# Kernel tuning notes

Hardware: AMD Instinct MI355X
Metric: run time of the kernel (lower is better)

The kernel has to match this reference:

```python
import jax, jax.numpy as jnp
import numpy as np
import itertools

NUM_HEADS = 8
KEY_DIM = 32
ATTN_D = 128  # attn_ratio * key_dim
BN_EPS = 1e-5


def _build_idxs(rx=16, rz=8, tn=1):
    points = list(itertools.product(range(rx), range(rx)))
    for i in range(tn):
        points += list(itertools.product(range(rx + rz * i, rx + rz * (i + 1)),
                                         range(rx + rz * i, rx + rz * (i + 1))))
    offsets = {}
    idxs = []
    for p1 in points:
        for p2 in points:
            off = (abs(p1[0] - p2[0]), abs(p1[1] - p2[1]))
            if off not in offsets:
                offsets[off] = len(offsets)
            idxs.append(offsets[off])
    N = len(points)
    return np.asarray(idxs, dtype=np.int64).reshape(N, N), len(offsets)


def _bn_train(x2d, gamma, beta):
    # BatchNorm1d in training mode: batch mean / biased variance over dim 0
    m = jnp.mean(x2d, axis=0)
    v = jnp.var(x2d, axis=0)
    return (x2d - m) * jax.lax.rsqrt(v + BN_EPS) * gamma + beta


def setup_inputs() -> dict:
    key = jax.random.key(0)
    ks = jax.random.split(key, 4)
    idxs_np, n_off = _build_idxs()  # (320,320), 560
    B, N, C = 128, idxs_np.shape[0], 256
    h = NUM_HEADS * (2 * KEY_DIM + ATTN_D)  # 1536
    dh = NUM_HEADS * ATTN_D  # 1024
    return {
        "x": jax.random.normal(ks[0], (B, N, C), dtype=jnp.float32),
        "Wqkv": jax.random.normal(ks[1], (h, C), dtype=jnp.float32) * 0.02,
        "g1": jnp.ones((h,), jnp.float32),
        "b1": jnp.zeros((h,), jnp.float32),
        "ab": jax.random.normal(ks[2], (NUM_HEADS, n_off), dtype=jnp.float32) * 0.02,
        "Wproj": jax.random.normal(ks[3], (C, dh), dtype=jnp.float32) * 0.02,
        "g2": jnp.ones((C,), jnp.float32),
        "b2": jnp.zeros((C,), jnp.float32),
        "idxs": jnp.asarray(idxs_np),
    }


def reference(x, Wqkv, g1, b1, ab, Wproj, g2, b2, idxs):
    B, N, C = x.shape
    scale = KEY_DIM ** -0.5
    # qkv projection (Linear no-bias) + BatchNorm1d over flattened (B*N, h)
    qkv = jnp.einsum('bnc,hc->bnh', x, Wqkv)
    qkv = _bn_train(qkv.reshape(B * N, -1), g1, b1).reshape(B, N, NUM_HEADS, 2 * KEY_DIM + ATTN_D)
    q = qkv[..., :KEY_DIM]
    k = qkv[..., KEY_DIM:2 * KEY_DIM]
    v = qkv[..., 2 * KEY_DIM:]
    bias = ab[:, idxs]  # gather -> (H, N, N)
    attn = jnp.einsum('bnhd,bmhd->bhnm', q, k) * scale + bias[None]
    attn = jax.nn.softmax(attn, axis=-1)
    out = jnp.einsum('bhnm,bmhd->bnhd', attn, v).reshape(B, N, NUM_HEADS * ATTN_D)
    out = jax.nn.gelu(out, approximate=False)  # activation() before proj
    out = jnp.einsum('bnd,cd->bnc', out, Wproj)
    out = _bn_train(out.reshape(B * N, -1), g2, b2).reshape(B, N, C)
    return out
```

## Files before the change

### kernel.cpp

```cpp
#include <hip/hip_runtime.h>
#include <hip/hip_bf16.h>

#define B_ 128
#define N_ 320
#define C_ 256
#define H_ 8
#define HQKV 1536
#define DH 1024
#define MROWS 40960
#define EPS 1e-5f
#define SCALE 0.17677669529663687f
#define LOG2E 1.4426950408889634f

typedef __attribute__((ext_vector_type(4))) float f32x4;
typedef __attribute__((ext_vector_type(8))) short short8_t;
typedef __attribute__((ext_vector_type(4))) short short4_t;

__device__ inline float bf2f(unsigned short u) { return __uint_as_float(((unsigned)u) << 16); }
__device__ inline unsigned short f2bf(float f) {
    unsigned u = __float_as_uint(f);
    u += 0x7FFF + ((u >> 16) & 1);
    return (unsigned short)(u >> 16);
}

__device__ inline float gelu_f(float v) {
    float v2 = v * v;
    float w = fmaf(v2, 0.044715f, 1.0f);
    float z = v * w * (-2.3022098f);
    float e = __builtin_amdgcn_exp2f(z);
    return v * __builtin_amdgcn_rcpf(1.0f + e);
}

#define GLD16(gp, lp)                                                                  \
    __builtin_amdgcn_global_load_lds((const __attribute__((address_space(1))) void*)(gp), \
                                     (__attribute__((address_space(3))) void*)(lp), 16, 0, 0)

__global__ void conv_all(const float* __restrict__ x, const float* __restrict__ wqkv,
                         const float* __restrict__ wproj, unsigned short* __restrict__ xb,
                         unsigned short* __restrict__ wqb, unsigned short* __restrict__ wpb) {
    int i = blockIdx.x * 256 + threadIdx.x;
    const float* src;
    unsigned short* dst;
    int off;
    if (i < 2621440) { src = x; dst = xb; off = i; }
    else if (i < 2719744) { src = wqkv; dst = wqb; off = i - 2621440; }
    else if (i < 2785280) { src = wproj; dst = wpb; off = i - 2719744; }
    else return;
    f32x4 v = ((const f32x4*)src)[off];
    short4_t o;
#pragma unroll
    for (int j = 0; j < 4; ++j) o[j] = (short)f2bf(v[j]);
    ((short4_t*)dst)[off] = o;
}

__global__ __launch_bounds__(256) void gemm_qkv(const unsigned short* __restrict__ A,
                                                const unsigned short* __restrict__ Bm,
                                                unsigned short* __restrict__ qkB,
                                                unsigned short* __restrict__ vT,
                                                float* __restrict__ sum1, float* __restrict__ sumsq1) {
    __shared__ unsigned short lA[128 * 32];
    __shared__ unsigned short lB[128 * 32];
    const int tid = threadIdx.x;
    const int lane = tid & 63, wid = tid >> 6;
    const int wm = wid >> 1, wn = wid & 1;
    const int lr = lane & 15, g = lane >> 4, lk = g * 8;
    const int m0 = blockIdx.y * 128, n0 = blockIdx.x * 128;
    const int wb0 = tid & 192;
    f32x4 acc[4][4] = {};
    for (int k0 = 0; k0 < 256; k0 += 32) {
        __syncthreads();
#pragma unroll
        for (int j = 0; j < 2; ++j) {
            int idx = j * 256 + tid;
            int wb = j * 256 + wb0;
            GLD16(&A[(size_t)(m0 + (idx >> 2)) * 256 + k0 + (idx & 3) * 8], &lA[(size_t)wb * 8]);
            GLD16(&Bm[(size_t)(n0 + (idx >> 2)) * 256 + k0 + (idx & 3) * 8], &lB[(size_t)wb * 8]);
        }
        __syncthreads();
        short8_t af[4], bfr[4];
#pragma unroll
        for (int i = 0; i < 4; ++i) af[i] = *(short8_t*)&lA[(wm * 64 + i * 16 + lr) * 32 + lk];
#pragma unroll
        for (int j = 0; j < 4; ++j) bfr[j] = *(short8_t*)&lB[(wn * 64 + j * 16 + lr) * 32 + lk];
#pragma unroll
        for (int i = 0; i < 4; ++i)
#pragma unroll
            for (int j = 0; j < 4; ++j)
                acc[i][j] = __builtin_amdgcn_mfma_f32_16x16x32_bf16(af[i], bfr[j], acc[i][j], 0, 0, 0);
    }
    int hhj[4], cmj[4];
#pragma unroll
    for (int j = 0; j < 4; ++j) {
        int col = n0 + wn * 64 + j * 16 + lr;
        hhj[j] = col / 192;
        cmj[j] = col - hhj[j] * 192;
    }
    float cs[4] = {0.f, 0.f, 0.f, 0.f}, css[4] = {0.f, 0.f, 0.f, 0.f};
#pragma unroll
    for (int i = 0; i < 4; ++i) {
        int rowbase = m0 + wm * 64 + i * 16 + g * 4;
        int bq = rowbase / 320;
        int n = rowbase - bq * 320;
#pragma unroll
        for (int j = 0; j < 4; ++j) {
            float v0 = acc[i][j][0], v1 = acc[i][j][1], v2 = acc[i][j][2], v3 = acc[i][j][3];
            cs[j] += (v0 + v1) + (v2 + v3);
            css[j] += (v0 * v0 + v1 * v1) + (v2 * v2 + v3 * v3);
            if (cmj[j] < 64) {
                unsigned short* qp = &qkB[((size_t)(bq * 8 + hhj[j]) * 320 + n) * 64 + cmj[j]];
                qp[0] = f2bf(v0); qp[64] = f2bf(v1); qp[128] = f2bf(v2); qp[192] = f2bf(v3);
            } else {
                short4_t o;
                o[0] = (short)f2bf(v0); o[1] = (short)f2bf(v1);
                o[2] = (short)f2bf(v2); o[3] = (short)f2bf(v3);
                *(short4_t*)&vT[((size_t)(bq * 8 + hhj[j]) * 128 + (cmj[j] - 64)) * 320 + n] = o;
            }
        }
    }
    __syncthreads();
    float* red_s = (float*)lA;
    float* red_ss = (float*)lB;
#pragma unroll
    for (int j = 0; j < 4; ++j) {
        int c = wn * 64 + j * 16 + lr;
        red_s[(wm * 4 + g) * 128 + c] = cs[j];
        red_ss[(wm * 4 + g) * 128 + c] = css[j];
    }
    __syncthreads();
    if (tid < 128) {
        float s = 0.f;
#pragma unroll
        for (int u = 0; u < 8; ++u) s += red_s[u * 128 + tid];
        atomicAdd(&sum1[n0 + tid], s);
    } else {
        int c = tid - 128;
        float s = 0.f;
#pragma unroll
        for (int u = 0; u < 8; ++u) s += red_ss[u * 128 + c];
        atomicAdd(&sumsq1[n0 + c], s);
    }
}

__global__ __launch_bounds__(256) void gemm_proj(const unsigned short* __restrict__ A,
                                                 const unsigned short* __restrict__ Bm,
                                                 float* __restrict__ Cout,
                                                 float* __restrict__ sum2, float* __restrict__ sumsq2) {
    __shared__ unsigned short lA[64 * 32];
    __shared__ unsigned short lB[128 * 32];
    const int tid = threadIdx.x;
    const int lane = tid & 63, wid = tid >> 6;
    const int wm = wid >> 1, wn = wid & 1;
    const int lr = lane & 15, g = lane >> 4, lk = g * 8;
    const int m0 = blockIdx.y * 64, n0 = blockIdx.x * 128;
    const int wb0 = tid & 192;
    f32x4 acc[2][4] = {};
    for (int k0 = 0; k0 < 1024; k0 += 32) {
        __syncthreads();
        GLD16(&A[(size_t)(m0 + (tid >> 2)) * 1024 + k0 + (tid & 3) * 8], &lA[(size_t)wb0 * 8]);
        GLD16(&Bm[(size_t)(n0 + (tid >> 2)) * 1024 + k0 + (tid & 3) * 8], &lB[(size_t)wb0 * 8]);
        GLD16(&Bm[(size_t)(n0 + 64 + (tid >> 2)) * 1024 + k0 + (tid & 3) * 8], &lB[2048 + (size_t)wb0 * 8]);
        __syncthreads();
        short8_t af[2], bfr[4];
#pragma unroll
        for (int i = 0; i < 2; ++i) af[i] = *(short8_t*)&lA[(wm * 32 + i * 16 + lr) * 32 + lk];
#pragma unroll
        for (int j = 0; j < 4; ++j) bfr[j] = *(short8_t*)&lB[(wn * 64 + j * 16 + lr) * 32 + lk];
#pragma unroll
        for (int i = 0; i < 2; ++i)
#pragma unroll
            for (int j = 0; j < 4; ++j)
                acc[i][j] = __builtin_amdgcn_mfma_f32_16x16x32_bf16(af[i], bfr[j], acc[i][j], 0, 0, 0);
    }
    float cs[4] = {0.f, 0.f, 0.f, 0.f}, css[4] = {0.f, 0.f, 0.f, 0.f};
#pragma unroll
    for (int i = 0; i < 2; ++i) {
#pragma unroll
        for (int r = 0; r < 4; ++r) {
            int row = m0 + wm * 32 + i * 16 + g * 4 + r;
#pragma unroll
            for (int j = 0; j < 4; ++j) {
                float val = acc[i][j][r];
                cs[j] += val;
                css[j] += val * val;
                Cout[(size_t)row * 256 + n0 + wn * 64 + j * 16 + lr] = val;
            }
        }
    }
    __syncthreads();
    float* red_s = (float*)lB;
    float* red_ss = (float*)lB + 1024;
#pragma unroll
    for (int j = 0; j < 4; ++j) {
        int c = wn * 64 + j * 16 + lr;
        red_s[(wm * 4 + g) * 128 + c] = cs[j];
        red_ss[(wm * 4 + g) * 128 + c] = css[j];
    }
    __syncthreads();
    if (tid < 128) {
        float s = 0.f;
#pragma unroll
        for (int u = 0; u < 8; ++u) s += red_s[u * 128 + tid];
        atomicAdd(&sum2[n0 + tid], s);
    } else {
        int c = tid - 128;
        float s = 0.f;
#pragma unroll
        for (int u = 0; u < 8; ++u) s += red_ss[u * 128 + c];
        atomicAdd(&sumsq2[n0 + c], s);
    }
}

__global__ void bn_finalize(const float* __restrict__ sum, const float* __restrict__ sumsq,
                            const float* __restrict__ g, const float* __restrict__ b,
                            float* __restrict__ scale, float* __restrict__ shift, int C, float invM) {
    int c = blockIdx.x * 256 + threadIdx.x;
    if (c < C) {
        float mean = sum[c] * invM;
        float var = sumsq[c] * invM - mean * mean;
        float sc = g[c] * rsqrtf(var + EPS);
        scale[c] = sc;
        shift[c] = b[c] - mean * sc;
    }
}

__global__ void prep_w(const float* __restrict__ scale1, const float* __restrict__ shift1,
                       float* __restrict__ wq, float* __restrict__ w2) {
    int c = threadIdx.x;
    if (c < 256) {
        int h = c >> 5, cc = c & 31;
        int qch = h * 192 + cc, kch = qch + 32;
        wq[c] = scale1[qch] * scale1[kch] * (SCALE * LOG2E);
        w2[c] = shift1[qch] * scale1[kch] * (SCALE * LOG2E);
    }
}

__global__ void uk_kernel(const unsigned short* __restrict__ qkB, const float* __restrict__ w2,
                          float* __restrict__ uk) {
    int idx = blockIdx.x * 256 + threadIdx.x;
    if (idx < 128 * 8 * 320) {
        int bh = idx / 320;
        int h = bh & 7;
        const unsigned short* kp = &qkB[(size_t)idx * 64 + 32];
        float s = 0.f;
#pragma unroll
        for (int c4 = 0; c4 < 4; ++c4) {
            short8_t kk = *(const short8_t*)&kp[c4 * 8];
#pragma unroll
            for (int j = 0; j < 8; ++j) s += bf2f((unsigned short)kk[j]) * w2[(h << 5) + c4 * 8 + j];
        }
        uk[idx] = s;
    }
}

__global__ void bias_build(const float* __restrict__ ab, const int* __restrict__ idxs,
                           unsigned short* __restrict__ biasb, int n_off) {
    int i = blockIdx.x * 256 + threadIdx.x;
    if (i < H_ * N_ * N_) {
        int h = i / (N_ * N_);
        int r = i % (N_ * N_);
        biasb[i] = f2bf(ab[h * n_off + idxs[r]] * LOG2E);
    }
}

__global__ __launch_bounds__(256) void attn_kernel(const unsigned short* __restrict__ qkB,
                                                   const unsigned short* __restrict__ vT,
                                                   const float* __restrict__ wq,
                                                   const float* __restrict__ uk,
                                                   const unsigned short* __restrict__ biasb,
                                                   const float* __restrict__ scale1,
                                                   const float* __restrict__ shift1,
                                                   unsigned short* __restrict__ attnout) {
    __shared__ unsigned short Plds[4][10][16][40];
    __shared__ float sums[64];
    const int tid = threadIdx.x;
    const int lane = tid & 63, wid = tid >> 6;
    const int lr = lane & 15, g = lane >> 4;
    const int h = blockIdx.x;
    const int b = blockIdx.y / 5, qt = blockIdx.y % 5;
    const int bh = b * 8 + h;

    int qrow = qt * 64 + wid * 16 + lr;
    short8_t qraw = *(const short8_t*)&qkB[((size_t)bh * 320 + qrow) * 64 + g * 8];
    short8_t aq;
#pragma unroll
    for (int j = 0; j < 8; ++j)
        aq[j] = (short)f2bf(bf2f((unsigned short)qraw[j]) * wq[(h << 5) + g * 8 + j]);

    const unsigned short* Kbase = &qkB[(size_t)bh * 320 * 64 + 32 + g * 8];
    f32x4 sacc[20];
#pragma unroll
    for (int t = 0; t < 20; ++t) {
        short8_t bk = *(const short8_t*)&Kbase[(size_t)(t * 16 + lr) * 64];
        f32x4 z = {};
        sacc[t] = __builtin_amdgcn_mfma_f32_16x16x32_bf16(aq, bk, z, 0, 0, 0);
    }

    const int nloc0 = qt * 64 + wid * 16 + g * 4;
    const unsigned short* biasrow = &biasb[(size_t)h * 102400];
    const float* ukrow = &uk[(size_t)bh * 320];
    float sumr[4] = {0.f, 0.f, 0.f, 0.f};
#pragma unroll
    for (int t = 0; t < 20; ++t) {
        float ukv = ukrow[t * 16 + lr];
#pragma unroll
        for (int r = 0; r < 4; ++r) {
            float s = sacc[t][r] + ukv + bf2f(biasrow[(size_t)(nloc0 + r) * 320 + t * 16 + lr]);
            float p = __builtin_amdgcn_exp2f(s);
            sumr[r] += p;
            Plds[wid][t >> 1][g * 4 + r][(t & 1) * 16 + lr] = f2bf(p);
        }
    }
#pragma unroll
    for (int r = 0; r < 4; ++r) {
#pragma unroll
        for (int ms = 1; ms < 16; ms <<= 1) sumr[r] += __shfl_xor(sumr[r], ms);
        if (lr == 0) sums[wid * 16 + g * 4 + r] = sumr[r];
    }
    __syncthreads();

    const unsigned short* Vb = &vT[(size_t)bh * 128 * 320 + g * 8];
    f32x4 oacc[4][2] = {};
#pragma unroll
    for (int t = 0; t < 10; ++t) {
        short8_t bv0 = *(const short8_t*)&Vb[(size_t)(wid * 32 + lr) * 320 + t * 32];
        short8_t bv1 = *(const short8_t*)&Vb[(size_t)(wid * 32 + 16 + lr) * 320 + t * 32];
#pragma unroll
        for (int qw = 0; qw < 4; ++qw) {
            short8_t ap = *(short8_t*)&Plds[qw][t][lr][g * 8];
            oacc[qw][0] = __builtin_amdgcn_mfma_f32_16x16x32_bf16(ap, bv0, oacc[qw][0], 0, 0, 0);
            oacc[qw][1] = __builtin_amdgcn_mfma_f32_16x16x32_bf16(ap, bv1, oacc[qw][1], 0, 0, 0);
        }
    }

    float svv[2], tvv[2];
#pragma unroll
    for (int dtl = 0; dtl < 2; ++dtl) {
        int ch = h * 192 + 64 + wid * 32 + dtl * 16 + lr;
        svv[dtl] = scale1[ch];
        tvv[dtl] = shift1[ch];
    }
#pragma unroll
    for (int qw = 0; qw < 4; ++qw) {
#pragma unroll
        for (int r = 0; r < 4; ++r) {
            float inv = __builtin_amdgcn_rcpf(sums[qw * 16 + g * 4 + r]);
            size_t nrow = (size_t)b * 320 + qt * 64 + qw * 16 + g * 4 + r;
#pragma unroll
            for (int dtl = 0; dtl < 2; ++dtl) {
                float v = oacc[qw][dtl][r] * inv * svv[dtl] + tvv[dtl];
                attnout[nrow * 1024 + h * 128 + wid * 32 + dtl * 16 + lr] = f2bf(gelu_f(v));
            }
        }
    }
}

__global__ void bn_apply(float* __restrict__ out, const float* __restrict__ scale,
                         const float* __restrict__ shift) {
    int i = blockIdx.x * 256 + threadIdx.x;
    const int total = MROWS * C_ / 4;
    for (; i < total; i += gridDim.x * 256) {
        f32x4 v = *(const f32x4*)&out[(size_t)i * 4];
        int c = (i * 4) & 255;
        f32x4 o;
#pragma unroll
        for (int j = 0; j < 4; ++j) o[j] = v[j] * scale[c + j] + shift[c + j];
        *(f32x4*)&out[(size_t)i * 4] = o;
    }
}

extern "C" void kernel_launch(void* const* d_in, const int* in_sizes, int n_in,
                              void* d_out, int out_size, void* d_ws, size_t ws_size,
                              hipStream_t stream) {
    const float* x = (const float*)d_in[0];
    const float* Wqkv = (const float*)d_in[1];
    const float* g1 = (const float*)d_in[2];
    const float* b1 = (const float*)d_in[3];
    const float* ab = (const float*)d_in[4];
    const float* Wproj = (const float*)d_in[5];
    const float* g2 = (const float*)d_in[6];
    const float* b2 = (const float*)d_in[7];
    const int* idxs = (const int*)d_in[8];
    const int n_off = in_sizes[4] / H_;

    char* ws = (char*)d_ws;
    unsigned short* qkB = (unsigned short*)ws;
    unsigned short* vT = (unsigned short*)(ws + 41943040);
    unsigned short* attnout = (unsigned short*)(ws + 125829120);
    unsigned short* xb = attnout;
    unsigned short* biasb = (unsigned short*)(ws + 209715200);
    float* uk = (float*)(ws + 212992000);
    unsigned short* wqb = (unsigned short*)(ws + 214302720);
    unsigned short* wpb = (unsigned short*)(ws + 215089152);
    float* stats = (float*)(ws + 215613440);
    float* sum1 = stats;
    float* sumsq1 = stats + 1536;
    float* sum2 = stats + 3072;
    float* sumsq2 = sum2 + 256;
    float* scale1 = sumsq2 + 256;
    float* shift1 = scale1 + 1536;
    float* scale2 = shift1 + 1536;
    float* shift2 = scale2 + 256;
    float* wq = shift2 + 256;
    float* w2 = wq + 256;

    hipMemsetAsync(stats, 0, 3584 * 4, stream);
    conv_all<<<dim3(10880), 256, 0, stream>>>(x, Wqkv, Wproj, xb, wqb, wpb);
    bias_build<<<dim3(3200), 256, 0, stream>>>(ab, idxs, biasb, n_off);
    gemm_qkv<<<dim3(12, 320), 256, 0, stream>>>(xb, wqb, qkB, vT, sum1, sumsq1);
    bn_finalize<<<dim3(6), 256, 0, stream>>>(sum1, sumsq1, g1, b1, scale1, shift1, 1536, 1.0f / MROWS);
    prep_w<<<dim3(1), 256, 0, stream>>>(scale1, shift1, wq, w2);
    uk_kernel<<<dim3(1280), 256, 0, stream>>>(qkB, w2, uk);
    attn_kernel<<<dim3(8, 640), 256, 0, stream>>>(qkB, vT, wq, uk, biasb, scale1, shift1, attnout);
    gemm_proj<<<dim3(2, 640), 256, 0, stream>>>(attnout, wpb, (float*)d_out, sum2, sumsq2);
    bn_finalize<<<dim3(1), 256, 0, stream>>>(sum2, sumsq2, g2, b2, scale2, shift2, 256, 1.0f / MROWS);
    bn_apply<<<dim3(2048), 256, 0, stream>>>((float*)d_out, scale2, shift2);
}
```

Baseline: 301.7 us.

## Split attention softmax/PV into two key halves and vectorize bias loads

The attention kernel now processes the 320 keys in two halves of 160, so each wave keeps fewer score accumulators live and uses half the P tile in LDS. Launch bounds request 5 blocks per CU. The bias table is stored as fp32 and read as float4 along the query dimension, relying on the relative-position bias being symmetric. Probabilities are converted to bf16 in pairs. The cost is an extra __syncthreads per half, and the bias table doubles in size, adding global memory traffic.

```diff
diff --git a/kernel.cpp b/kernel.cpp
--- a/kernel.cpp
+++ b/kernel.cpp
@@ -21,6 +21,10 @@
     unsigned u = __float_as_uint(f);
     u += 0x7FFF + ((u >> 16) & 1);
     return (unsigned short)(u >> 16);
+}
+__device__ inline unsigned int f2bf2(float a, float b) {
+    __hip_bfloat162 h2 = __float22bfloat162_rn(make_float2(a, b));
+    return *(unsigned int*)&h2;
 }
 
 __device__ inline float gelu_f(float v) {
@@ -253,24 +257,24 @@
 }
 
 __global__ void bias_build(const float* __restrict__ ab, const int* __restrict__ idxs,
-                           unsigned short* __restrict__ biasb, int n_off) {
+                           float* __restrict__ biasf, int n_off) {
     int i = blockIdx.x * 256 + threadIdx.x;
     if (i < H_ * N_ * N_) {
         int h = i / (N_ * N_);
         int r = i % (N_ * N_);
-        biasb[i] = f2bf(ab[h * n_off + idxs[r]] * LOG2E);
-    }
-}
-
-__global__ __launch_bounds__(256) void attn_kernel(const unsigned short* __restrict__ qkB,
-                                                   const unsigned short* __restrict__ vT,
-                                                   const float* __restrict__ wq,
-                                                   const float* __restrict__ uk,
-                                                   const unsigned short* __restrict__ biasb,
-                                                   const float* __restrict__ scale1,
-                                                   const float* __restrict__ shift1,
-                                                   unsigned short* __restrict__ attnout) {
-    __shared__ unsigned short Plds[4][10][16][40];
+        biasf[i] = ab[h * n_off + idxs[r]] * LOG2E;
+    }
+}
+
+__global__ __launch_bounds__(256, 5) void attn_kernel(const unsigned short* __restrict__ qkB,
+                                                      const unsigned short* __restrict__ vT,
+                                                      const float* __restrict__ wq,
+                                                      const float* __restrict__ uk,
+                                                      const float* __restrict__ biasf,
+                                                      const float* __restrict__ scale1,
+                                                      const float* __restrict__ shift1,
+                                                      unsigned short* __restrict__ attnout) {
+    __shared__ unsigned short Plds[4][5][16][40];
     __shared__ float sums[64];
     const int tid = threadIdx.x;
     const int lane = tid & 63, wid = tid >> 6;
@@ -287,50 +291,65 @@
         aq[j] = (short)f2bf(bf2f((unsigned short)qraw[j]) * wq[(h << 5) + g * 8 + j]);
 
     const unsigned short* Kbase = &qkB[(size_t)bh * 320 * 64 + 32 + g * 8];
-    f32x4 sacc[20];
-#pragma unroll
-    for (int t = 0; t < 20; ++t) {
-        short8_t bk = *(const short8_t*)&Kbase[(size_t)(t * 16 + lr) * 64];
-        f32x4 z = {};
-        sacc[t] = __builtin_amdgcn_mfma_f32_16x16x32_bf16(aq, bk, z, 0, 0, 0);
-    }
-
     const int nloc0 = qt * 64 + wid * 16 + g * 4;
-    const unsigned short* biasrow = &biasb[(size_t)h * 102400];
+    const float* biasT = &biasf[(size_t)h * 102400];
     const float* ukrow = &uk[(size_t)bh * 320];
+    const unsigned short* Vb = &vT[(size_t)bh * 128 * 320 + g * 8];
+
     float sumr[4] = {0.f, 0.f, 0.f, 0.f};
-#pragma unroll
-    for (int t = 0; t < 20; ++t) {
-        float ukv = ukrow[t * 16 + lr];
-#pragma unroll
-        for (int r = 0; r < 4; ++r) {
-            float s = sacc[t][r] + ukv + bf2f(biasrow[(size_t)(nloc0 + r) * 320 + t * 16 + lr]);
-            float p = __builtin_amdgcn_exp2f(s);
-            sumr[r] += p;
-            Plds[wid][t >> 1][g * 4 + r][(t & 1) * 16 + lr] = f2bf(p);
-        }
-    }
+    f32x4 oacc[4][2] = {};
+#pragma unroll
+    for (int half = 0; half < 2; ++half) {
+        const int mbase = half * 160;
+        f32x4 sacc[10];
+#pragma unroll
+        for (int t = 0; t < 10; ++t) {
+            short8_t bk = *(const short8_t*)&Kbase[(size_t)(mbase + t * 16 + lr) * 64];
+            f32x4 z = {};
+            sacc[t] = __builtin_amdgcn_mfma_f32_16x16x32_bf16(aq, bk, z, 0, 0, 0);
+        }
+#pragma unroll
+        for (int t = 0; t < 10; ++t) {
+            int m = mbase + t * 16 + lr;
+            f32x4 b4 = *(const f32x4*)&biasT[(size_t)m * 320 + nloc0];
+            float ukv = ukrow[m];
+            float p0 = __builtin_amdgcn_exp2f(sacc[t][0] + ukv + b4[0]);
+            float p1 = __builtin_amdgcn_exp2f(sacc[t][1] + ukv + b4[1]);
+            float p2 = __builtin_amdgcn_exp2f(sacc[t][2] + ukv + b4[2]);
+            float p3 = __builtin_amdgcn_exp2f(sacc[t][3] + ukv + b4[3]);
+            sumr[0] += p0; sumr[1] += p1; sumr[2] += p2; sumr[3] += p3;
+            unsigned pk01 = f2bf2(p0, p1), pk23 = f2bf2(p2, p3);
+            unsigned short* pp = &Plds[wid][t >> 1][g * 4][(t & 1) * 16 + lr];
+            pp[0] = (unsigned short)pk01;
+            pp[40] = (unsigned short)(pk01 >> 16);
+            pp[80] = (unsigned short)pk23;
+            pp[120] = (unsigned short)(pk23 >> 16);
+        }
+        __syncthreads();
+#pragma unroll
+        for (int t = 0; t < 5; ++t) {
+            short8_t bv0 = *(const short8_t*)&Vb[(size_t)(wid * 32 + lr) * 320 + mbase + t * 32];
+            short8_t bv1 = *(const short8_t*)&Vb[(size_t)(wid * 32 + 16 + lr) * 320 + mbase + t * 32];
+#pragma unroll
+            for (int qw = 0; qw < 4; ++qw) {
+                short8_t ap = *(short8_t*)&Plds[qw][t][lr][g * 8];
+                oacc[qw][0] = __builtin_amdgcn_mfma_f32_16x16x32_bf16(ap, bv0, oacc[qw][0], 0, 0, 0);
+                oacc[qw][1] = __builtin_amdgcn_mfma_f32_16x16x32_bf16(ap, bv1, oacc[qw][1], 0, 0, 0);
+            }
+        }
+        __syncthreads();
+    }
+
 #pragma unroll
     for (int r = 0; r < 4; ++r) {
 #pragma unroll
         for (int ms = 1; ms < 16; ms <<= 1) sumr[r] += __shfl_xor(sumr[r], ms);
-        if (lr == 0) sums[wid * 16 + g * 4 + r] = sumr[r];
+    }
+    if (lr == 0) {
+#pragma unroll
+        for (int r = 0; r < 4; ++r) sums[wid * 16 + g * 4 + r] = sumr[r];
     }
     __syncthreads();
-
-    const unsigned short* Vb = &vT[(size_t)bh * 128 * 320 + g * 8];
-    f32x4 oacc[4][2] = {};
-#pragma unroll
-    for (int t = 0; t < 10; ++t) {
-        short8_t bv0 = *(const short8_t*)&Vb[(size_t)(wid * 32 + lr) * 320 + t * 32];
-        short8_t bv1 = *(const short8_t*)&Vb[(size_t)(wid * 32 + 16 + lr) * 320 + t * 32];
-#pragma unroll
-        for (int qw = 0; qw < 4; ++qw) {
-            short8_t ap = *(short8_t*)&Plds[qw][t][lr][g * 8];
-            oacc[qw][0] = __builtin_amdgcn_mfma_f32_16x16x32_bf16(ap, bv0, oacc[qw][0], 0, 0, 0);
-            oacc[qw][1] = __builtin_amdgcn_mfma_f32_16x16x32_bf16(ap, bv1, oacc[qw][1], 0, 0, 0);
-        }
-    }
 
     float svv[2], tvv[2];
 #pragma unroll
@@ -387,7 +406,7 @@
     unsigned short* vT = (unsigned short*)(ws + 41943040);
     unsigned short* attnout = (unsigned short*)(ws + 125829120);
     unsigned short* xb = attnout;
-    unsigned short* biasb = (unsigned short*)(ws + 209715200);
+    float* biasf = (float*)(ws + 209715200);
     float* uk = (float*)(ws + 212992000);
     unsigned short* wqb = (unsigned short*)(ws + 214302720);
     unsigned short* wpb = (unsigned short*)(ws + 215089152);
@@ -405,12 +424,12 @@
 
     hipMemsetAsync(stats, 0, 3584 * 4, stream);
     conv_all<<<dim3(10880), 256, 0, stream>>>(x, Wqkv, Wproj, xb, wqb, wpb);
-    bias_build<<<dim3(3200), 256, 0, stream>>>(ab, idxs, biasb, n_off);
+    bias_build<<<dim3(3200), 256, 0, stream>>>(ab, idxs, biasf, n_off);
     gemm_qkv<<<dim3(12, 320), 256, 0, stream>>>(xb, wqb, qkB, vT, sum1, sumsq1);
     bn_finalize<<<dim3(6), 256, 0, stream>>>(sum1, sumsq1, g1, b1, scale1, shift1, 1536, 1.0f / MROWS);
     prep_w<<<dim3(1), 256, 0, stream>>>(scale1, shift1, wq, w2);
     uk_kernel<<<dim3(1280), 256, 0, stream>>>(qkB, w2, uk);
-    attn_kernel<<<dim3(8, 640), 256, 0, stream>>>(qkB, vT, wq, uk, biasb, scale1, shift1, attnout);
+    attn_kernel<<<dim3(8, 640), 256, 0, stream>>>(qkB, vT, wq, uk, biasf, scale1, shift1, attnout);
     gemm_proj<<<dim3(2, 640), 256, 0, stream>>>(attnout, wpb, (float*)d_out, sum2, sumsq2);
     bn_finalize<<<dim3(1), 256, 0, stream>>>(sum2, sumsq2, g2, b2, scale2, shift2, 256, 1.0f / MROWS);
     bn_apply<<<dim3(2048), 256, 0, stream>>>((float*)d_out, scale2, shift2);
```

New measurement: 336.7 us. 1.12x slower.

## Transpose attention score MFMA for vectorized bias loads; remap QKV GEMM block order

Applied to the files above, without the earlier changes.

The attention score MFMA operands are swapped so each lane holds four consecutive key columns for a single query row. This allows float4 loads of bias and uk, packed bf16x2 stores of P into LDS, and a row-sum reduction that needs only two shuffles instead of four sets of four. The relative-position bias is now stored as fp32, which doubles that buffer's size and read traffic but removes per-element bf16 decode. Separately, the QKV GEMM remaps block IDs so consecutive blocks within a chiplet share tiles, aiming for better L2 reuse.

```diff
diff --git a/kernel.cpp b/kernel.cpp
--- a/kernel.cpp
+++ b/kernel.cpp
@@ -21,6 +21,10 @@
     unsigned u = __float_as_uint(f);
     u += 0x7FFF + ((u >> 16) & 1);
     return (unsigned short)(u >> 16);
+}
+__device__ inline unsigned int f2bf2(float a, float b) {
+    __hip_bfloat162 h2 = __float22bfloat162_rn(make_float2(a, b));
+    return *(unsigned int*)&h2;
 }
 
 __device__ inline float gelu_f(float v) {
@@ -64,7 +68,9 @@
     const int lane = tid & 63, wid = tid >> 6;
     const int wm = wid >> 1, wn = wid & 1;
     const int lr = lane & 15, g = lane >> 4, lk = g * 8;
-    const int m0 = blockIdx.y * 128, n0 = blockIdx.x * 128;
+    const int orig = blockIdx.y * 12 + blockIdx.x;
+    const int id2 = (orig & 7) * 480 + (orig >> 3);
+    const int m0 = (id2 / 12) * 128, n0 = (id2 % 12) * 128;
     const int wb0 = tid & 192;
     f32x4 acc[4][4] = {};
     for (int k0 = 0; k0 < 256; k0 += 32) {
@@ -253,12 +259,12 @@
 }
 
 __global__ void bias_build(const float* __restrict__ ab, const int* __restrict__ idxs,
-                           unsigned short* __restrict__ biasb, int n_off) {
+                           float* __restrict__ biasf, int n_off) {
     int i = blockIdx.x * 256 + threadIdx.x;
     if (i < H_ * N_ * N_) {
         int h = i / (N_ * N_);
         int r = i % (N_ * N_);
-        biasb[i] = f2bf(ab[h * n_off + idxs[r]] * LOG2E);
+        biasf[i] = ab[h * n_off + idxs[r]] * LOG2E;
     }
 }
 
@@ -266,7 +272,7 @@
                                                    const unsigned short* __restrict__ vT,
                                                    const float* __restrict__ wq,
                                                    const float* __restrict__ uk,
-                                                   const unsigned short* __restrict__ biasb,
+                                                   const float* __restrict__ biasf,
                                                    const float* __restrict__ scale1,
                                                    const float* __restrict__ shift1,
                                                    unsigned short* __restrict__ attnout) {
@@ -279,7 +285,7 @@
     const int b = blockIdx.y / 5, qt = blockIdx.y % 5;
     const int bh = b * 8 + h;
 
-    int qrow = qt * 64 + wid * 16 + lr;
+    const int qrow = qt * 64 + wid * 16 + lr;
     short8_t qraw = *(const short8_t*)&qkB[((size_t)bh * 320 + qrow) * 64 + g * 8];
     short8_t aq;
 #pragma unroll
@@ -292,30 +298,28 @@
     for (int t = 0; t < 20; ++t) {
         short8_t bk = *(const short8_t*)&Kbase[(size_t)(t * 16 + lr) * 64];
         f32x4 z = {};
-        sacc[t] = __builtin_amdgcn_mfma_f32_16x16x32_bf16(aq, bk, z, 0, 0, 0);
-    }
-
-    const int nloc0 = qt * 64 + wid * 16 + g * 4;
-    const unsigned short* biasrow = &biasb[(size_t)h * 102400];
+        sacc[t] = __builtin_amdgcn_mfma_f32_16x16x32_bf16(bk, aq, z, 0, 0, 0);
+    }
+
+    const float* brow = &biasf[(size_t)h * 102400 + (size_t)qrow * 320];
     const float* ukrow = &uk[(size_t)bh * 320];
-    float sumr[4] = {0.f, 0.f, 0.f, 0.f};
+    float sumr = 0.f;
 #pragma unroll
     for (int t = 0; t < 20; ++t) {
-        float ukv = ukrow[t * 16 + lr];
-#pragma unroll
-        for (int r = 0; r < 4; ++r) {
-            float s = sacc[t][r] + ukv + bf2f(biasrow[(size_t)(nloc0 + r) * 320 + t * 16 + lr]);
-            float p = __builtin_amdgcn_exp2f(s);
-            sumr[r] += p;
-            Plds[wid][t >> 1][g * 4 + r][(t & 1) * 16 + lr] = f2bf(p);
-        }
-    }
-#pragma unroll
-    for (int r = 0; r < 4; ++r) {
-#pragma unroll
-        for (int ms = 1; ms < 16; ms <<= 1) sumr[r] += __shfl_xor(sumr[r], ms);
-        if (lr == 0) sums[wid * 16 + g * 4 + r] = sumr[r];
-    }
+        int mb = t * 16 + g * 4;
+        f32x4 b4 = *(const f32x4*)&brow[mb];
+        f32x4 uk4 = *(const f32x4*)&ukrow[mb];
+        float p0 = __builtin_amdgcn_exp2f(sacc[t][0] + uk4[0] + b4[0]);
+        float p1 = __builtin_amdgcn_exp2f(sacc[t][1] + uk4[1] + b4[1]);
+        float p2 = __builtin_amdgcn_exp2f(sacc[t][2] + uk4[2] + b4[2]);
+        float p3 = __builtin_amdgcn_exp2f(sacc[t][3] + uk4[3] + b4[3]);
+        sumr += (p0 + p1) + (p2 + p3);
+        *(uint2*)&Plds[wid][t >> 1][lr][((t & 1) << 4) + (g << 2)] =
+            make_uint2(f2bf2(p0, p1), f2bf2(p2, p3));
+    }
+    sumr += __shfl_xor(sumr, 16);
+    sumr += __shfl_xor(sumr, 32);
+    if (lane < 16) sums[wid * 16 + lr] = sumr;
     __syncthreads();
 
     const unsigned short* Vb = &vT[(size_t)bh * 128 * 320 + g * 8];
@@ -387,7 +391,7 @@
     unsigned short* vT = (unsigned short*)(ws + 41943040);
     unsigned short* attnout = (unsigned short*)(ws + 125829120);
     unsigned short* xb = attnout;
-    unsigned short* biasb = (unsigned short*)(ws + 209715200);
+    float* biasf = (float*)(ws + 209715200);
     float* uk = (float*)(ws + 212992000);
     unsigned short* wqb = (unsigned short*)(ws + 214302720);
     unsigned short* wpb = (unsigned short*)(ws + 215089152);
@@ -405,12 +409,12 @@
 
     hipMemsetAsync(stats, 0, 3584 * 4, stream);
     conv_all<<<dim3(10880), 256, 0, stream>>>(x, Wqkv, Wproj, xb, wqb, wpb);
-    bias_build<<<dim3(3200), 256, 0, stream>>>(ab, idxs, biasb, n_off);
+    bias_build<<<dim3(3200), 256, 0, stream>>>(ab, idxs, biasf, n_off);
     gemm_qkv<<<dim3(12, 320), 256, 0, stream>>>(xb, wqb, qkB, vT, sum1, sumsq1);
     bn_finalize<<<dim3(6), 256, 0, stream>>>(sum1, sumsq1, g1, b1, scale1, shift1, 1536, 1.0f / MROWS);
     prep_w<<<dim3(1), 256, 0, stream>>>(scale1, shift1, wq, w2);
     uk_kernel<<<dim3(1280), 256, 0, stream>>>(qkB, w2, uk);
-    attn_kernel<<<dim3(8, 640), 256, 0, stream>>>(qkB, vT, wq, uk, biasb, scale1, shift1, attnout);
+    attn_kernel<<<dim3(8, 640), 256, 0, stream>>>(qkB, vT, wq, uk, biasf, scale1, shift1, attnout);
     gemm_proj<<<dim3(2, 640), 256, 0, stream>>>(attnout, wpb, (float*)d_out, sum2, sumsq2);
     bn_finalize<<<dim3(1), 256, 0, stream>>>(sum2, sumsq2, g2, b2, scale2, shift2, 256, 1.0f / MROWS);
     bn_apply<<<dim3(2048), 256, 0, stream>>>((float*)d_out, scale2, shift2);
```

New measurement: 329.0 us. +9.1%, slower.
